# Kernel tuning notes

Hardware: AMD Instinct MI355X
Metric: run time of the kernel (lower is better)

## Reference

```python
import jax, jax.numpy as jnp
import numpy as np

LN_EPS = 1e-5  # torch nn.LayerNorm default eps


def _layernorm(x, g, b):
    m = jnp.mean(x, -1, keepdims=True)
    v = jnp.mean((x - m) ** 2, -1, keepdims=True)
    return (x - m) / jnp.sqrt(v + LN_EPS) * g + b


def _dw_causal_conv(x, w, bias=None):
    # x: (B, L, C); w: (C, K) depthwise kernels; causal via left-pad K-1
    C = x.shape[-1]
    K = w.shape[-1]
    xt = jnp.swapaxes(x, 1, 2)                       # (B, C, L)
    xp = jnp.pad(xt, ((0, 0), (0, 0), (K - 1, 0)))
    y = jax.lax.conv_general_dilated(
        xp, w[:, None, :], (1,), 'VALID',
        feature_group_count=C, dimension_numbers=('NCH', 'OIH', 'NCH'))
    if bias is not None:
        y = y + bias[None, :, None]
    return jnp.swapaxes(y, 1, 2)                     # (B, L, C)


def _s4d(x, Bp, Cp, log_dt, Dp):
    # Diagonal SSM: kernel K[l] = sum_n C[n]*dB[n]*dA[n]^l, shared across channels
    L, Dm = x.shape[1], x.shape[2]
    n = Bp.shape[0]
    A = -jnp.arange(1, n + 1, dtype=x.dtype)
    dt = jnp.clip(jnp.exp(log_dt), 1e-4, 1.0)
    dA = jnp.exp(jnp.clip(dt * A, -10.0, 10.0))                  # (n,)
    dB = (dA - 1.0) / jnp.minimum(A, -1e-4) * Bp                 # (n,)
    pows = dA[:, None] ** jnp.arange(L, dtype=x.dtype)[None, :]  # (n, L)
    Kk = jnp.nan_to_num((Cp * dB) @ pows, nan=0.0, posinf=0.0, neginf=0.0)  # (L,)
    y = _dw_causal_conv(x, jnp.broadcast_to(Kk[None, :], (Dm, L)))
    return y + Dp * x


def _mamba_block(x, g, b, W_in, cw, cb, sB, sC, ldt, sD, W_out, rs):
    res = x
    h = _layernorm(x, g, b)
    xz = h @ W_in.T                                  # (B, L, 2*d_inner)
    xp, z = jnp.split(xz, 2, axis=-1)
    xc = _dw_causal_conv(xp, cw, cb)                 # depthwise causal conv, k=4
    y = _s4d(xc, sB, sC, ldt, sD) * jax.nn.sigmoid(z)
    y = y @ W_out.T
    return res + jnp.clip(rs, 0.0, 1.5) * y          # dropout is identity in eval


def _forward(spatial_tokens_init, pos_embed, ln_g, ln_b, W_in, conv_w, conv_b,
             ssm_B, ssm_C, log_dt, ssm_D, W_out, res_scale, fin_g, fin_b,
             imp_W1, imp_b1, imp_W2, imp_b2, tex_W, tex_b, edge_W, edge_b,
             str_W, str_b):
    x = spatial_tokens_init + pos_embed
    for i in range(ln_g.shape[0]):  # fixed small layer count
        x = _mamba_block(x, ln_g[i], ln_b[i], W_in[i], conv_w[i], conv_b[i],
                         ssm_B[i], ssm_C[i], log_dt[i], ssm_D[i], W_out[i],
                         res_scale[i])
    tokens = _layernorm(x, fin_g, fin_b)
    # F.normalize(dim=-1, eps=1e-6)
    tn = tokens / jnp.maximum(jnp.sqrt(jnp.sum(tokens ** 2, -1, keepdims=True)), 1e-6)
    h = jax.nn.gelu(tn @ imp_W1.T + imp_b1, approximate=False)
    logits = (h @ imp_W2.T + imp_b2)[..., 0]
    w = jax.nn.softmax(logits, axis=-1)
    feats = jnp.sum(tokens * w[..., None], axis=1)
    return (feats,
            feats @ tex_W.T + tex_b,
            feats @ edge_W.T + edge_b,
            feats @ str_W.T + str_b,
            tokens, w)


B, N, D, DI, NL, NS, KC, DH = 512, 256, 128, 256, 4, 16, 4, 64
H = D // 2


def setup_inputs() -> dict:
    ks = jax.random.split(jax.random.key(0), 26)
    r = lambda k, sh, s=0.02: jax.random.normal(k, sh, dtype=jnp.float32) * s
    inp = {
        'spatial_tokens_init': jax.random.normal(ks[0], (B, N, D), dtype=jnp.float32),
        'pos_embed': r(ks[1], (1, N, D)),
        'ln_g': jnp.ones((NL, D), jnp.float32),
        'ln_b': jnp.zeros((NL, D), jnp.float32),
        'W_in': r(ks[2], (NL, 2 * DI, D)),
        'conv_w': r(ks[3], (NL, DI, KC), 0.2),
        'conv_b': r(ks[4], (NL, DI), 0.02),
        'ssm_B': r(ks[5], (NL, NS)),
        'ssm_C': r(ks[6], (NL, NS)),
        'log_dt': jax.random.uniform(ks[7], (NL,), jnp.float32,
                                     minval=float(np.log(1e-3)), maxval=float(np.log(0.1))),
        'ssm_D': jnp.zeros((NL,), jnp.float32),
        'W_out': r(ks[8], (NL, D, DI)),
        'res_scale': jnp.ones((NL,), jnp.float32),
        'fin_g': jnp.ones((D,), jnp.float32),
        'fin_b': jnp.zeros((D,), jnp.float32),
        'imp_W1': r(ks[9], (H, D)),
        'imp_b1': jnp.zeros((H,), jnp.float32),
        'imp_W2': r(ks[10], (1, H)),
        'imp_b2': jnp.zeros((1,), jnp.float32),
        'tex_W': r(ks[11], (DH, D)),
        'tex_b': jnp.zeros((DH,), jnp.float32),
        'edge_W': r(ks[12], (DH, D)),
        'edge_b': jnp.zeros((DH,), jnp.float32),
        'str_W': r(ks[13], (DH, D)),
        'str_b': jnp.zeros((DH,), jnp.float32),
    }
    return inp


def reference(spatial_tokens_init, pos_embed, ln_g, ln_b, W_in, conv_w, conv_b,
              ssm_B, ssm_C, log_dt, ssm_D, W_out, res_scale, fin_g, fin_b,
              imp_W1, imp_b1, imp_W2, imp_b2, tex_W, tex_b, edge_W, edge_b,
              str_W, str_b):
    return _forward(spatial_tokens_init, pos_embed, ln_g, ln_b, W_in, conv_w,
                    conv_b, ssm_B, ssm_C, log_dt, ssm_D, W_out, res_scale,
                    fin_g, fin_b, imp_W1, imp_b1, imp_W2, imp_b2, tex_W, tex_b,
                    edge_W, edge_b, str_W, str_b)
```

## Files before the change

kernel.cpp:

```cpp
#include <hip/hip_runtime.h>
#include <hip/hip_bf16.h>


typedef __bf16 bf16_8 __attribute__((ext_vector_type(8)));
typedef __bf16 bf16_4 __attribute__((ext_vector_type(4)));
typedef float  f32_4  __attribute__((ext_vector_type(4)));

#define LDKC 72

__global__ __launch_bounds__(256) void prep_kernel(const float* __restrict__ win,
                                                   const float* __restrict__ wout,
                                                   const float* __restrict__ w1,
                                                   __bf16* __restrict__ win16,
                                                   __bf16* __restrict__ wout16,
                                                   __bf16* __restrict__ w116) {
    int i = blockIdx.x * 256 + threadIdx.x;
    if (i < 4 * 512 * 128) win16[i] = (__bf16)win[i];
    if (i < 4 * 128 * 256) wout16[i] = (__bf16)wout[i];
    if (i < 64 * 128)      w116[i]  = (__bf16)w1[i];
}

__global__ __launch_bounds__(256) void build_T_kernel(const float* __restrict__ Bp,
                                                      const float* __restrict__ Cp,
                                                      const float* __restrict__ ldt,
                                                      const float* __restrict__ Dpv,
                                                      __bf16* __restrict__ Tg,
                                                      float* __restrict__ Rg) {
    __shared__ float rsum[4];
    int layer = blockIdx.y, l = blockIdx.x, j = threadIdx.x;
    int d = l - j;
    float val = 0.0f;
    if (d >= 0) {
        float dt = expf(ldt[layer]);
        dt = fminf(fmaxf(dt, 1e-4f), 1.0f);
        #pragma unroll
        for (int n = 0; n < 16; ++n) {
            float A = -(float)(n + 1);
            float e = fminf(fmaxf(dt * A, -10.0f), 10.0f);
            float dA = expf(e);
            float dB = (dA - 1.0f) / A * Bp[layer * 16 + n];
            val += Cp[layer * 16 + n] * dB * expf(e * (float)d);
        }
        if (d == 0) val += Dpv[layer];
    }
    __bf16 bv = (__bf16)val;
    Tg[layer * 65536 + l * 256 + j] = bv;
    float fv = (float)bv;
    #pragma unroll
    for (int o = 32; o; o >>= 1) fv += __shfl_xor(fv, o);
    int lane = j & 63, wave = j >> 6;
    if (lane == 0) rsum[wave] = fv;
    __syncthreads();
    if (j == 0) Rg[layer * 256 + l] = rsum[0] + rsum[1] + rsum[2] + rsum[3];
}

__global__ __launch_bounds__(256) void ln_first_kernel(const float* __restrict__ init,
                                                       const float* __restrict__ pos,
                                                       const float* __restrict__ g,
                                                       const float* __restrict__ bta,
                                                       float* __restrict__ x,
                                                       __bf16* __restrict__ h) {
    int wave = threadIdx.x >> 6, lane = threadIdx.x & 63;
    long tok = (long)blockIdx.x * 4 + wave;
    const float* xr = init + tok * 128;
    const float* pr = pos + (tok & 255) * 128;
    float v0 = xr[lane] + pr[lane];
    float v1 = xr[lane + 64] + pr[lane + 64];
    x[tok * 128 + lane]      = v0;
    x[tok * 128 + lane + 64] = v1;
    float s = v0 + v1, ss = v0 * v0 + v1 * v1;
    #pragma unroll
    for (int o = 32; o; o >>= 1) { s += __shfl_xor(s, o); ss += __shfl_xor(ss, o); }
    float m = s * (1.0f / 128.0f);
    float var = ss * (1.0f / 128.0f) - m * m;
    float r = rsqrtf(var + 1e-5f);
    __bf16* hr = h + tok * 128;
    hr[lane]      = (__bf16)((v0 - m) * r * g[lane]      + bta[lane]);
    hr[lane + 64] = (__bf16)((v1 - m) * r * g[lane + 64] + bta[lane + 64]);
}

__global__ __launch_bounds__(256) void gemm1_kernel(const __bf16* __restrict__ hmat,
                                                    const __bf16* __restrict__ win,
                                                    __bf16* __restrict__ xpt,
                                                    __bf16* __restrict__ z) {
    __shared__ __bf16 As[128 * LDKC];
    __shared__ __bf16 Bs[128 * LDKC];
    int tid = threadIdx.x;
    long m0 = (long)blockIdx.x * 128;
    int n0 = blockIdx.y * 128;
    int wave = tid >> 6, lane = tid & 63;
    int wm = wave >> 1, wn = wave & 1;
    int lrow = lane & 15, lk = (lane >> 4) * 8;
    f32_4 acc[4][4] = {};

    for (int kc = 0; kc < 2; ++kc) {
        const __bf16* asrc = hmat + m0 * 128 + kc * 64;
        const __bf16* bsrc = win + (long)n0 * 128 + kc * 64;
        #pragma unroll
        for (int i = 0; i < 4; ++i) {
            int idx = tid + i * 256;
            int row = idx >> 3, c4 = idx & 7;
            uint4 va = *(const uint4*)(asrc + row * 128 + c4 * 8);
            *(uint4*)(As + row * LDKC + c4 * 8) = va;
            uint4 vb = *(const uint4*)(bsrc + row * 128 + c4 * 8);
            *(uint4*)(Bs + row * LDKC + c4 * 8) = vb;
        }
        __syncthreads();
        #pragma unroll
        for (int kk = 0; kk < 64; kk += 32) {
            bf16_8 a[4], b[4];
            #pragma unroll
            for (int mt = 0; mt < 4; ++mt)
                a[mt] = *(const bf16_8*)(As + (wm * 64 + mt * 16 + lrow) * LDKC + kk + lk);
            #pragma unroll
            for (int nt = 0; nt < 4; ++nt)
                b[nt] = *(const bf16_8*)(Bs + (wn * 64 + nt * 16 + lrow) * LDKC + kk + lk);
            #pragma unroll
            for (int mt = 0; mt < 4; ++mt)
                #pragma unroll
                for (int nt = 0; nt < 4; ++nt)
                    acc[mt][nt] = __builtin_amdgcn_mfma_f32_16x16x32_bf16(
                        a[mt], b[nt], acc[mt][nt], 0, 0, 0);
        }
        __syncthreads();
    }

    int row_base = (lane >> 4) * 4;
    int col = lane & 15;
    if (n0 < 256) {
        #pragma unroll
        for (int mt = 0; mt < 4; ++mt) {
            long mg = m0 + wm * 64 + mt * 16 + row_base;
            int b = (int)(mg >> 8), l = (int)(mg & 255);
            #pragma unroll
            for (int nt = 0; nt < 4; ++nt) {
                int ng = n0 + wn * 64 + nt * 16 + col;
                bf16_4 o;
                #pragma unroll
                for (int r = 0; r < 4; ++r) o[r] = (__bf16)acc[mt][nt][r];
                *(bf16_4*)(xpt + (long)b * 65536 + (long)ng * 256 + l) = o;
            }
        }
    } else {
        int ncol0 = n0 - 256;
        #pragma unroll
        for (int mt = 0; mt < 4; ++mt) {
            long mg = m0 + wm * 64 + mt * 16 + row_base;
            #pragma unroll
            for (int nt = 0; nt < 4; ++nt) {
                int ng = ncol0 + wn * 64 + nt * 16 + col;
                #pragma unroll
                for (int r = 0; r < 4; ++r)
                    z[(mg + r) * 256 + ng] = (__bf16)acc[mt][nt][r];
            }
        }
    }
}

__global__ __launch_bounds__(512) void ssm_gemm_kernel(const __bf16* __restrict__ xct,
                                                       __bf16* __restrict__ zy,
                                                       const __bf16* __restrict__ Tg,
                                                       const float* __restrict__ Rg,
                                                       const float* __restrict__ cw,
                                                       const float* __restrict__ cb) {
    __shared__ __bf16 As[256 * LDKC];
    __shared__ __bf16 Bs[128 * LDKC];
    __shared__ float  bnd[3][128];
    __shared__ float  Rs[256];
    int tid = threadIdx.x;
    int batch = blockIdx.x >> 1;
    int ntile = blockIdx.x & 1;
    int c0 = ntile * 128;

    int wave = tid >> 6, lane = tid & 63;
    int wm = wave >> 2, wn = wave & 3;
    int lrow = lane & 15, lk = (lane >> 4) * 8;
    int quad = lane >> 4;
    f32_4 acc[8][2] = {};
    const __bf16* bsrc0 = xct + (long)batch * 65536 + (long)c0 * 256;

    if (tid < 256) Rs[tid] = Rg[tid];

    for (int kc = 0; kc < 4; ++kc) {
        int j0 = kc * 64;
        #pragma unroll
        for (int i = 0; i < 4; ++i) {
            int idx = tid + i * 512;
            int row = idx >> 3, c4 = idx & 7;
            uint4 va = *(const uint4*)(Tg + row * 256 + j0 + c4 * 8);
            *(uint4*)(As + row * LDKC + c4 * 8) = va;
        }
        #pragma unroll
        for (int i = 0; i < 2; ++i) {
            int idx = tid + i * 512;
            int row = idx >> 3, c4 = idx & 7;
            uint4 vb = *(const uint4*)(bsrc0 + (long)row * 256 + j0 + c4 * 8);
            *(uint4*)(Bs + row * LDKC + c4 * 8) = vb;
        }
        __syncthreads();
        #pragma unroll
        for (int kk = 0; kk < 64; kk += 32) {
            bf16_8 b0 = *(const bf16_8*)(Bs + (wn * 32 + lrow) * LDKC + kk + lk);
            bf16_8 b1 = *(const bf16_8*)(Bs + (wn * 32 + 16 + lrow) * LDKC + kk + lk);
            #pragma unroll
            for (int mt = 0; mt < 8; ++mt) {
                bf16_8 a = *(const bf16_8*)(As + (wm * 128 + mt * 16 + lrow) * LDKC + kk + lk);
                acc[mt][0] = __builtin_amdgcn_mfma_f32_16x16x32_bf16(a, b0, acc[mt][0], 0, 0, 0);
                acc[mt][1] = __builtin_amdgcn_mfma_f32_16x16x32_bf16(a, b1, acc[mt][1], 0, 0, 0);
            }
        }
        __syncthreads();
    }

    if (wm == 0 && quad == 3) {
        #pragma unroll
        for (int nt = 0; nt < 2; ++nt) {
            int colb = wn * 32 + nt * 16 + lrow;
            bnd[0][colb] = acc[7][nt][1];
            bnd[1][colb] = acc[7][nt][2];
            bnd[2][colb] = acc[7][nt][3];
        }
    }
    __syncthreads();

    float4 wv[2]; float cbv[2];
    #pragma unroll
    for (int nt = 0; nt < 2; ++nt) {
        int cg = c0 + wn * 32 + nt * 16 + lrow;
        wv[nt] = *(const float4*)(cw + cg * 4);
        cbv[nt] = cb[cg];
    }
    int src = (lane + 48) & 63;

    #pragma unroll
    for (int mt = 0; mt < 8; ++mt) {
        int lbase = wm * 128 + mt * 16 + quad * 4;
        int mp = mt > 0 ? mt - 1 : 0;
        float R0 = Rs[lbase], R1 = Rs[lbase + 1], R2 = Rs[lbase + 2], R3 = Rs[lbase + 3];
        #pragma unroll
        for (int nt = 0; nt < 2; ++nt) {
            int colb = wn * 32 + nt * 16 + lrow;
            int cg = c0 + colb;
            float s1 = __shfl(acc[mt][nt][3], src);
            float s2 = __shfl(acc[mt][nt][2], src);
            float s3 = __shfl(acc[mt][nt][1], src);
            float t1, t2, t3;
            if (mt == 0) {
                if (wm == 1) { t1 = bnd[2][colb]; t2 = bnd[1][colb]; t3 = bnd[0][colb]; }
                else         { t1 = 0.0f; t2 = 0.0f; t3 = 0.0f; }
            } else {
                t1 = __shfl(acc[mp][nt][3], src);
                t2 = __shfl(acc[mp][nt][2], src);
                t3 = __shfl(acc[mp][nt][1], src);
            }
            float pm1 = quad ? s1 : t1;
            float pm2 = quad ? s2 : t2;
            float pm3 = quad ? s3 : t3;
            float p0 = acc[mt][nt][0], p1 = acc[mt][nt][1];
            float p2 = acc[mt][nt][2], p3 = acc[mt][nt][3];
            float y0 = wv[nt].x * pm3 + wv[nt].y * pm2 + wv[nt].z * pm1 + wv[nt].w * p0 + cbv[nt] * R0;
            float y1 = wv[nt].x * pm2 + wv[nt].y * pm1 + wv[nt].z * p0  + wv[nt].w * p1 + cbv[nt] * R1;
            float y2 = wv[nt].x * pm1 + wv[nt].y * p0  + wv[nt].z * p1  + wv[nt].w * p2 + cbv[nt] * R2;
            float y3 = wv[nt].x * p0  + wv[nt].y * p1  + wv[nt].z * p2  + wv[nt].w * p3 + cbv[nt] * R3;
            long base = (long)batch * 65536 + (long)lbase * 256 + cg;
            float z0 = (float)zy[base];
            float z1 = (float)zy[base + 256];
            float z2 = (float)zy[base + 512];
            float z3 = (float)zy[base + 768];
            zy[base]       = (__bf16)(y0 / (1.0f + expf(-z0)));
            zy[base + 256] = (__bf16)(y1 / (1.0f + expf(-z1)));
            zy[base + 512] = (__bf16)(y2 / (1.0f + expf(-z2)));
            zy[base + 768] = (__bf16)(y3 / (1.0f + expf(-z3)));
        }
    }
}

__global__ __launch_bounds__(256) void gemm2_kernel(const __bf16* __restrict__ y,
                                                    const __bf16* __restrict__ wout,
                                                    float* __restrict__ x,
                                                    const float* __restrict__ rs_p,
                                                    const float* __restrict__ g,
                                                    const float* __restrict__ bta,
                                                    __bf16* __restrict__ hout,
                                                    float* __restrict__ tokens_out,
                                                    int final_mode) {
    __shared__ __bf16 As[128 * LDKC];
    __shared__ __bf16 Bs[128 * LDKC];
    __shared__ float s_sum[128][2];
    __shared__ float s_ssq[128][2];
    int tid = threadIdx.x;
    long m0 = (long)blockIdx.x * 128;
    int wave = tid >> 6, lane = tid & 63;
    int wm = wave >> 1, wn = wave & 1;
    int lrow = lane & 15, lk = (lane >> 4) * 8;
    f32_4 acc[4][4] = {};

    for (int kc = 0; kc < 4; ++kc) {
        const __bf16* asrc = y + m0 * 256 + kc * 64;
        const __bf16* bsrc = wout + kc * 64;
        #pragma unroll
        for (int i = 0; i < 4; ++i) {
            int idx = tid + i * 256;
            int row = idx >> 3, c4 = idx & 7;
            uint4 va = *(const uint4*)(asrc + row * 256 + c4 * 8);
            *(uint4*)(As + row * LDKC + c4 * 8) = va;
            uint4 vb = *(const uint4*)(bsrc + row * 256 + c4 * 8);
            *(uint4*)(Bs + row * LDKC + c4 * 8) = vb;
        }
        __syncthreads();
        #pragma unroll
        for (int kk = 0; kk < 64; kk += 32) {
            bf16_8 a[4], b[4];
            #pragma unroll
            for (int mt = 0; mt < 4; ++mt)
                a[mt] = *(const bf16_8*)(As + (wm * 64 + mt * 16 + lrow) * LDKC + kk + lk);
            #pragma unroll
            for (int nt = 0; nt < 4; ++nt)
                b[nt] = *(const bf16_8*)(Bs + (wn * 64 + nt * 16 + lrow) * LDKC + kk + lk);
            #pragma unroll
            for (int mt = 0; mt < 4; ++mt)
                #pragma unroll
                for (int nt = 0; nt < 4; ++nt)
                    acc[mt][nt] = __builtin_amdgcn_mfma_f32_16x16x32_bf16(
                        a[mt], b[nt], acc[mt][nt], 0, 0, 0);
        }
        __syncthreads();
    }

    float rs = rs_p[0];
    rs = fminf(fmaxf(rs, 0.0f), 1.5f);
    int quad = lane >> 4;
    int col = lane & 15;

    #pragma unroll
    for (int mt = 0; mt < 4; ++mt) {
        long mg = m0 + wm * 64 + mt * 16 + quad * 4;
        int tb = wm * 64 + mt * 16 + quad * 4;
        #pragma unroll
        for (int r = 0; r < 4; ++r) {
            float s = 0.0f, ss = 0.0f;
            #pragma unroll
            for (int nt = 0; nt < 4; ++nt) {
                int d = wn * 64 + nt * 16 + col;
                float xv = x[(mg + r) * 128 + d] + rs * acc[mt][nt][r];
                acc[mt][nt][r] = xv;
                s += xv; ss += xv * xv;
            }
            #pragma unroll
            for (int o = 8; o; o >>= 1) { s += __shfl_xor(s, o); ss += __shfl_xor(ss, o); }
            if (col == 0) {
                s_sum[tb + r][wn] = s;
                s_ssq[tb + r][wn] = ss;
            }
        }
    }
    __syncthreads();

    #pragma unroll
    for (int mt = 0; mt < 4; ++mt) {
        long mg = m0 + wm * 64 + mt * 16 + quad * 4;
        int tb = wm * 64 + mt * 16 + quad * 4;
        #pragma unroll
        for (int r = 0; r < 4; ++r) {
            float s  = s_sum[tb + r][0] + s_sum[tb + r][1];
            float ss = s_ssq[tb + r][0] + s_ssq[tb + r][1];
            float m = s * (1.0f / 128.0f);
            float var = ss * (1.0f / 128.0f) - m * m;
            float rstd = rsqrtf(var + 1e-5f);
            #pragma unroll
            for (int nt = 0; nt < 4; ++nt) {
                int d = wn * 64 + nt * 16 + col;
                float xv = acc[mt][nt][r];
                x[(mg + r) * 128 + d] = xv;
                float t = (xv - m) * rstd * g[d] + bta[d];
                if (!final_mode) {
                    hout[(mg + r) * 128 + d] = (__bf16)t;
                } else {
                    tokens_out[(mg + r) * 128 + d] = t;
                }
            }
        }
    }
}

__global__ __launch_bounds__(256) void l2n_kernel(const float* __restrict__ tokens,
                                                  __bf16* __restrict__ tn) {
    int wave = threadIdx.x >> 6, lane = threadIdx.x & 63;
    long tok = (long)blockIdx.x * 4 + wave;
    const float* tr = tokens + tok * 128;
    float t0 = tr[lane], t1 = tr[lane + 64];
    float q = t0 * t0 + t1 * t1;
    #pragma unroll
    for (int o = 32; o; o >>= 1) q += __shfl_xor(q, o);
    float inv = 1.0f / fmaxf(sqrtf(q), 1e-6f);
    tn[tok * 128 + lane]      = (__bf16)(t0 * inv);
    tn[tok * 128 + lane + 64] = (__bf16)(t1 * inv);
}

#define LDA 136
__global__ __launch_bounds__(256) void mlp_kernel(const __bf16* __restrict__ tn,
                                                  const __bf16* __restrict__ w1b,
                                                  const float* __restrict__ b1,
                                                  const float* __restrict__ W2,
                                                  const float* __restrict__ b2,
                                                  float* __restrict__ logits) {
    __shared__ __bf16 As[128 * LDA];
    __shared__ __bf16 Bs[64 * LDA];
    int tid = threadIdx.x;
    long m0 = (long)blockIdx.x * 128;
    const __bf16* asrc = tn + m0 * 128;
    #pragma unroll
    for (int i = 0; i < 8; ++i) {
        int idx = tid + i * 256;
        int row = idx >> 4, c = idx & 15;
        uint4 v = *(const uint4*)(asrc + row * 128 + c * 8);
        *(uint4*)(As + row * LDA + c * 8) = v;
    }
    #pragma unroll
    for (int i = 0; i < 4; ++i) {
        int idx = tid + i * 256;
        int row = idx >> 4, c = idx & 15;
        uint4 v = *(const uint4*)(w1b + row * 128 + c * 8);
        *(uint4*)(Bs + row * LDA + c * 8) = v;
    }
    __syncthreads();

    int wave = tid >> 6, lane = tid & 63;
    int lrow = lane & 15, lk = (lane >> 4) * 8;
    f32_4 acc[2][4] = {};
    #pragma unroll
    for (int kk = 0; kk < 128; kk += 32) {
        bf16_8 a[2], b[4];
        #pragma unroll
        for (int mt = 0; mt < 2; ++mt)
            a[mt] = *(const bf16_8*)(As + (wave * 32 + mt * 16 + lrow) * LDA + kk + lk);
        #pragma unroll
        for (int nt = 0; nt < 4; ++nt)
            b[nt] = *(const bf16_8*)(Bs + (nt * 16 + lrow) * LDA + kk + lk);
        #pragma unroll
        for (int mt = 0; mt < 2; ++mt)
            #pragma unroll
            for (int nt = 0; nt < 4; ++nt)
                acc[mt][nt] = __builtin_amdgcn_mfma_f32_16x16x32_bf16(
                    a[mt], b[nt], acc[mt][nt], 0, 0, 0);
    }

    int col = lane & 15, quad = lane >> 4;
    float b2v = b2[0];
    #pragma unroll
    for (int mt = 0; mt < 2; ++mt) {
        #pragma unroll
        for (int r = 0; r < 4; ++r) {
            float p = 0.0f;
            #pragma unroll
            for (int nt = 0; nt < 4; ++nt) {
                int jx = nt * 16 + col;
                float a = acc[mt][nt][r] + b1[jx];
                float gl = 0.5f * a * (1.0f + erff(a * 0.70710678118654752f));
                p += gl * W2[jx];
            }
            #pragma unroll
            for (int o = 8; o; o >>= 1) p += __shfl_xor(p, o);
            if (col == 0) {
                long tok = m0 + wave * 32 + mt * 16 + quad * 4 + r;
                logits[tok] = p + b2v;
            }
        }
    }
}

__global__ __launch_bounds__(256) void head_kernel(const float* __restrict__ tokens,
                                                   const float* __restrict__ logits,
                                                   const float* __restrict__ texW,
                                                   const float* __restrict__ texb,
                                                   const float* __restrict__ edgeW,
                                                   const float* __restrict__ edgeb,
                                                   const float* __restrict__ strW,
                                                   const float* __restrict__ strb,
                                                   float* __restrict__ feats_out,
                                                   float* __restrict__ tex_out,
                                                   float* __restrict__ edge_out,
                                                   float* __restrict__ str_out,
                                                   float* __restrict__ w_out) {
    __shared__ float wsm[256];
    __shared__ float red[8];
    __shared__ float feats_s[128];
    int b = blockIdx.x, tid = threadIdx.x;
    int lane = tid & 63, wave = tid >> 6;
    float lg = logits[(long)b * 256 + tid];
    float mx = lg;
    #pragma unroll
    for (int o = 32; o; o >>= 1) mx = fmaxf(mx, __shfl_xor(mx, o));
    if (lane == 0) red[wave] = mx;
    __syncthreads();
    float bm = fmaxf(fmaxf(red[0], red[1]), fmaxf(red[2], red[3]));
    float e = expf(lg - bm);
    float se = e;
    #pragma unroll
    for (int o = 32; o; o >>= 1) se += __shfl_xor(se, o);
    if (lane == 0) red[4 + wave] = se;
    __syncthreads();
    float tot = red[4] + red[5] + red[6] + red[7];
    float w = e / tot;
    wsm[tid] = w;
    w_out[(long)b * 256 + tid] = w;
    __syncthreads();
    if (tid < 128) {
        float acc = 0.0f;
        const float* tb = tokens + (long)b * 256 * 128 + tid;
        #pragma unroll 4
        for (int l = 0; l < 256; ++l) acc += tb[l * 128] * wsm[l];
        feats_s[tid] = acc;
        feats_out[(long)b * 128 + tid] = acc;
    }
    __syncthreads();
    if (tid < 192) {
        int head = tid >> 6, j = tid & 63;
        const float* W  = head == 0 ? texW : (head == 1 ? edgeW : strW);
        const float* bi = head == 0 ? texb : (head == 1 ? edgeb : strb);
        float* outp     = head == 0 ? tex_out : (head == 1 ? edge_out : str_out);
        const float* wr = W + j * 128;
        float acc = 0.0f;
        #pragma unroll 8
        for (int k = 0; k < 128; ++k) acc += feats_s[k] * wr[k];
        outp[(long)b * 64 + j] = acc + bi[j];
    }
}

extern "C" void kernel_launch(void* const* d_in, const int* in_sizes, int n_in,
                              void* d_out, int out_size, void* d_ws, size_t ws_size,
                              hipStream_t stream) {
    const float* init   = (const float*)d_in[0];
    const float* pos    = (const float*)d_in[1];
    const float* ln_g   = (const float*)d_in[2];
    const float* ln_b   = (const float*)d_in[3];
    const float* W_in   = (const float*)d_in[4];
    const float* conv_w = (const float*)d_in[5];
    const float* conv_b = (const float*)d_in[6];
    const float* ssm_B  = (const float*)d_in[7];
    const float* ssm_C  = (const float*)d_in[8];
    const float* log_dt = (const float*)d_in[9];
    const float* ssm_D  = (const float*)d_in[10];
    const float* W_out  = (const float*)d_in[11];
    const float* res_sc = (const float*)d_in[12];
    const float* fin_g  = (const float*)d_in[13];
    const float* fin_b  = (const float*)d_in[14];
    const float* imp_W1 = (const float*)d_in[15];
    const float* imp_b1 = (const float*)d_in[16];
    const float* imp_W2 = (const float*)d_in[17];
    const float* imp_b2 = (const float*)d_in[18];
    const float* tex_W  = (const float*)d_in[19];
    const float* tex_b  = (const float*)d_in[20];
    const float* edge_W = (const float*)d_in[21];
    const float* edge_b = (const float*)d_in[22];
    const float* str_W  = (const float*)d_in[23];
    const float* str_b  = (const float*)d_in[24];

    float* out = (float*)d_out;
    char* ws = (char*)d_ws;
    float*  x      = (float*)ws;
    __bf16* xpt    = (__bf16*)(ws + 67108864);
    __bf16* zb     = (__bf16*)(ws + 134217728);
    __bf16* hb     = (__bf16*)(ws + 201326592);
    __bf16* win16  = (__bf16*)(ws + 234881024);
    __bf16* wout16 = (__bf16*)(ws + 235405312);
    float*  logits = (float*)(ws + 235667456);
    __bf16* w1b    = (__bf16*)(ws + 236191744);
    __bf16* Tg     = (__bf16*)(ws + 236208128);
    float*  Rg     = (float*)(ws + 236732416);

    float* tokens = out + 163840;

    prep_kernel<<<1024, 256, 0, stream>>>(W_in, W_out, imp_W1, win16, wout16, w1b);
    build_T_kernel<<<dim3(256, 4), 256, 0, stream>>>(ssm_B, ssm_C, log_dt, ssm_D, Tg, Rg);
    ln_first_kernel<<<32768, 256, 0, stream>>>(init, pos, ln_g, ln_b, x, hb);
    for (int l = 0; l < 4; ++l) {
        gemm1_kernel<<<dim3(1024, 4), 256, 0, stream>>>(hb, win16 + l * 65536, xpt, zb);
        ssm_gemm_kernel<<<1024, 512, 0, stream>>>(xpt, zb, Tg + l * 65536, Rg + l * 256,
                                                  conv_w + l * 1024, conv_b + l * 256);
        int fin = (l == 3);
        const float* gn = fin ? fin_g : ln_g + (l + 1) * 128;
        const float* bn = fin ? fin_b : ln_b + (l + 1) * 128;
        gemm2_kernel<<<1024, 256, 0, stream>>>(zb, wout16 + l * 32768, x, res_sc + l,
                                               gn, bn, hb, fin ? tokens : nullptr, fin);
    }
    __bf16* tn = hb;
    l2n_kernel<<<32768, 256, 0, stream>>>(tokens, tn);
    mlp_kernel<<<1024, 256, 0, stream>>>(tn, w1b, imp_b1, imp_W2, imp_b2, logits);
    head_kernel<<<512, 256, 0, stream>>>(tokens, logits, tex_W, tex_b, edge_W, edge_b,
                                         str_W, str_b, out, out + 65536, out + 98304,
                                         out + 131072, out + 16941056);
}
```

Baseline: 857.5 us.

## Use direct global-to-LDS loads with XOR swizzle and vectorize LN kernels

Replaces the register-staged global-to-shared tile copies in the three GEMM kernels with global_load_lds 16-byte direct loads into an unpadded, XOR-swizzled LDS layout, and adjusts the MFMA fragment reads to match the swizzle. The aim is to cut VGPR traffic and the extra LDS writes, and to avoid bank conflicts without padding. The first-layer LayerNorm and L2-normalize kernels are also vectorized to float4 with two tokens per wave, which halves the grid size. The risk is that the swizzle mapping or the per-lane LDS placement of global_load_lds is wrong, and the loads are still synchronous with no overlap.

```diff
diff --git a/kernel.cpp b/kernel.cpp
--- a/kernel.cpp
+++ b/kernel.cpp
@@ -6,7 +6,9 @@
 typedef __bf16 bf16_4 __attribute__((ext_vector_type(4)));
 typedef float  f32_4  __attribute__((ext_vector_type(4)));
 
-#define LDKC 72
+#define GLOAD16(src, dst) __builtin_amdgcn_global_load_lds( \
+    (const __attribute__((address_space(1))) void*)(src),   \
+    (__attribute__((address_space(3))) void*)(dst), 16, 0, 0)
 
 __global__ __launch_bounds__(256) void prep_kernel(const float* __restrict__ win,
                                                    const float* __restrict__ wout,
@@ -54,67 +56,73 @@
     if (j == 0) Rg[layer * 256 + l] = rsum[0] + rsum[1] + rsum[2] + rsum[3];
 }
 
-__global__ __launch_bounds__(256) void ln_first_kernel(const float* __restrict__ init,
-                                                       const float* __restrict__ pos,
+__global__ __launch_bounds__(256) void ln_first_kernel(const float4* __restrict__ init4,
+                                                       const float4* __restrict__ pos4,
                                                        const float* __restrict__ g,
                                                        const float* __restrict__ bta,
-                                                       float* __restrict__ x,
+                                                       float4* __restrict__ x4,
                                                        __bf16* __restrict__ h) {
-    int wave = threadIdx.x >> 6, lane = threadIdx.x & 63;
-    long tok = (long)blockIdx.x * 4 + wave;
-    const float* xr = init + tok * 128;
-    const float* pr = pos + (tok & 255) * 128;
-    float v0 = xr[lane] + pr[lane];
-    float v1 = xr[lane + 64] + pr[lane + 64];
-    x[tok * 128 + lane]      = v0;
-    x[tok * 128 + lane + 64] = v1;
-    float s = v0 + v1, ss = v0 * v0 + v1 * v1;
-    #pragma unroll
-    for (int o = 32; o; o >>= 1) { s += __shfl_xor(s, o); ss += __shfl_xor(ss, o); }
+    int tid = threadIdx.x;
+    int wave = tid >> 6, lane = tid & 63;
+    int half = lane >> 5, l32 = lane & 31;
+    long tok = (long)blockIdx.x * 8 + wave * 2 + half;
+    float4 v = init4[tok * 32 + l32];
+    float4 p = pos4[(tok & 255) * 32 + l32];
+    v.x += p.x; v.y += p.y; v.z += p.z; v.w += p.w;
+    x4[tok * 32 + l32] = v;
+    float s = v.x + v.y + v.z + v.w;
+    float ss = v.x * v.x + v.y * v.y + v.z * v.z + v.w * v.w;
+    #pragma unroll
+    for (int o = 16; o; o >>= 1) { s += __shfl_xor(s, o); ss += __shfl_xor(ss, o); }
     float m = s * (1.0f / 128.0f);
     float var = ss * (1.0f / 128.0f) - m * m;
     float r = rsqrtf(var + 1e-5f);
-    __bf16* hr = h + tok * 128;
-    hr[lane]      = (__bf16)((v0 - m) * r * g[lane]      + bta[lane]);
-    hr[lane + 64] = (__bf16)((v1 - m) * r * g[lane + 64] + bta[lane + 64]);
+    bf16_4 hv;
+    int d0 = l32 * 4;
+    hv[0] = (__bf16)((v.x - m) * r * g[d0]     + bta[d0]);
+    hv[1] = (__bf16)((v.y - m) * r * g[d0 + 1] + bta[d0 + 1]);
+    hv[2] = (__bf16)((v.z - m) * r * g[d0 + 2] + bta[d0 + 2]);
+    hv[3] = (__bf16)((v.w - m) * r * g[d0 + 3] + bta[d0 + 3]);
+    *(bf16_4*)(h + tok * 128 + d0) = hv;
 }
 
 __global__ __launch_bounds__(256) void gemm1_kernel(const __bf16* __restrict__ hmat,
                                                     const __bf16* __restrict__ win,
                                                     __bf16* __restrict__ xpt,
                                                     __bf16* __restrict__ z) {
-    __shared__ __bf16 As[128 * LDKC];
-    __shared__ __bf16 Bs[128 * LDKC];
+    __shared__ __align__(16) __bf16 As[128 * 64];
+    __shared__ __align__(16) __bf16 Bs[128 * 64];
     int tid = threadIdx.x;
     long m0 = (long)blockIdx.x * 128;
     int n0 = blockIdx.y * 128;
     int wave = tid >> 6, lane = tid & 63;
     int wm = wave >> 1, wn = wave & 1;
     int lrow = lane & 15, lk = (lane >> 4) * 8;
+    int r7 = lrow & 7;
+    int rl = lane >> 3, sl = lane & 7;
+    int scol = ((sl ^ rl) << 3);
     f32_4 acc[4][4] = {};
 
     for (int kc = 0; kc < 2; ++kc) {
         const __bf16* asrc = hmat + m0 * 128 + kc * 64;
         const __bf16* bsrc = win + (long)n0 * 128 + kc * 64;
         #pragma unroll
-        for (int i = 0; i < 4; ++i) {
-            int idx = tid + i * 256;
-            int row = idx >> 3, c4 = idx & 7;
-            uint4 va = *(const uint4*)(asrc + row * 128 + c4 * 8);
-            *(uint4*)(As + row * LDKC + c4 * 8) = va;
-            uint4 vb = *(const uint4*)(bsrc + row * 128 + c4 * 8);
-            *(uint4*)(Bs + row * LDKC + c4 * 8) = vb;
+        for (int j = 0; j < 4; ++j) {
+            int chunk = wave * 4 + j;
+            GLOAD16(asrc + (long)(chunk * 8 + rl) * 128 + scol, As + chunk * 512);
+            GLOAD16(bsrc + (long)(chunk * 8 + rl) * 128 + scol, Bs + chunk * 512);
         }
         __syncthreads();
         #pragma unroll
         for (int kk = 0; kk < 64; kk += 32) {
+            int sw = ((((kk + lk) >> 3) ^ r7) << 3);
             bf16_8 a[4], b[4];
             #pragma unroll
             for (int mt = 0; mt < 4; ++mt)
-                a[mt] = *(const bf16_8*)(As + (wm * 64 + mt * 16 + lrow) * LDKC + kk + lk);
+                a[mt] = *(const bf16_8*)(As + (wm * 64 + mt * 16 + lrow) * 64 + sw);
             #pragma unroll
             for (int nt = 0; nt < 4; ++nt)
-                b[nt] = *(const bf16_8*)(Bs + (wn * 64 + nt * 16 + lrow) * LDKC + kk + lk);
+                b[nt] = *(const bf16_8*)(Bs + (wn * 64 + nt * 16 + lrow) * 64 + sw);
             #pragma unroll
             for (int mt = 0; mt < 4; ++mt)
                 #pragma unroll
@@ -163,8 +171,8 @@
                                                        const float* __restrict__ Rg,
                                                        const float* __restrict__ cw,
                                                        const float* __restrict__ cb) {
-    __shared__ __bf16 As[256 * LDKC];
-    __shared__ __bf16 Bs[128 * LDKC];
+    __shared__ __align__(16) __bf16 As[256 * 64];
+    __shared__ __align__(16) __bf16 Bs[128 * 64];
     __shared__ float  bnd[3][128];
     __shared__ float  Rs[256];
     int tid = threadIdx.x;
@@ -175,7 +183,10 @@
     int wave = tid >> 6, lane = tid & 63;
     int wm = wave >> 2, wn = wave & 3;
     int lrow = lane & 15, lk = (lane >> 4) * 8;
+    int r7 = lrow & 7;
     int quad = lane >> 4;
+    int rl = lane >> 3, sl = lane & 7;
+    int scol = ((sl ^ rl) << 3);
     f32_4 acc[8][2] = {};
     const __bf16* bsrc0 = xct + (long)batch * 65536 + (long)c0 * 256;
 
@@ -183,28 +194,27 @@
 
     for (int kc = 0; kc < 4; ++kc) {
         int j0 = kc * 64;
-        #pragma unroll
-        for (int i = 0; i < 4; ++i) {
-            int idx = tid + i * 512;
-            int row = idx >> 3, c4 = idx & 7;
-            uint4 va = *(const uint4*)(Tg + row * 256 + j0 + c4 * 8);
-            *(uint4*)(As + row * LDKC + c4 * 8) = va;
-        }
-        #pragma unroll
-        for (int i = 0; i < 2; ++i) {
-            int idx = tid + i * 512;
-            int row = idx >> 3, c4 = idx & 7;
-            uint4 vb = *(const uint4*)(bsrc0 + (long)row * 256 + j0 + c4 * 8);
-            *(uint4*)(Bs + row * LDKC + c4 * 8) = vb;
+        const __bf16* asrc = Tg + j0;
+        const __bf16* bsrc = bsrc0 + j0;
+        #pragma unroll
+        for (int j = 0; j < 4; ++j) {
+            int chunk = wave * 4 + j;
+            GLOAD16(asrc + (long)(chunk * 8 + rl) * 256 + scol, As + chunk * 512);
+        }
+        #pragma unroll
+        for (int j = 0; j < 2; ++j) {
+            int chunk = wave * 2 + j;
+            GLOAD16(bsrc + (long)(chunk * 8 + rl) * 256 + scol, Bs + chunk * 512);
         }
         __syncthreads();
         #pragma unroll
         for (int kk = 0; kk < 64; kk += 32) {
-            bf16_8 b0 = *(const bf16_8*)(Bs + (wn * 32 + lrow) * LDKC + kk + lk);
-            bf16_8 b1 = *(const bf16_8*)(Bs + (wn * 32 + 16 + lrow) * LDKC + kk + lk);
+            int sw = ((((kk + lk) >> 3) ^ r7) << 3);
+            bf16_8 b0 = *(const bf16_8*)(Bs + (wn * 32 + lrow) * 64 + sw);
+            bf16_8 b1 = *(const bf16_8*)(Bs + (wn * 32 + 16 + lrow) * 64 + sw);
             #pragma unroll
             for (int mt = 0; mt < 8; ++mt) {
-                bf16_8 a = *(const bf16_8*)(As + (wm * 128 + mt * 16 + lrow) * LDKC + kk + lk);
+                bf16_8 a = *(const bf16_8*)(As + (wm * 128 + mt * 16 + lrow) * 64 + sw);
                 acc[mt][0] = __builtin_amdgcn_mfma_f32_16x16x32_bf16(a, b0, acc[mt][0], 0, 0, 0);
                 acc[mt][1] = __builtin_amdgcn_mfma_f32_16x16x32_bf16(a, b1, acc[mt][1], 0, 0, 0);
             }
@@ -284,8 +294,8 @@
                                                     __bf16* __restrict__ hout,
                                                     float* __restrict__ tokens_out,
                                                     int final_mode) {
-    __shared__ __bf16 As[128 * LDKC];
-    __shared__ __bf16 Bs[128 * LDKC];
+    __shared__ __align__(16) __bf16 As[128 * 64];
+    __shared__ __align__(16) __bf16 Bs[128 * 64];
     __shared__ float s_sum[128][2];
     __shared__ float s_ssq[128][2];
     int tid = threadIdx.x;
@@ -293,30 +303,31 @@
     int wave = tid >> 6, lane = tid & 63;
     int wm = wave >> 1, wn = wave & 1;
     int lrow = lane & 15, lk = (lane >> 4) * 8;
+    int r7 = lrow & 7;
+    int rl = lane >> 3, sl = lane & 7;
+    int scol = ((sl ^ rl) << 3);
     f32_4 acc[4][4] = {};
 
     for (int kc = 0; kc < 4; ++kc) {
         const __bf16* asrc = y + m0 * 256 + kc * 64;
         const __bf16* bsrc = wout + kc * 64;
         #pragma unroll
-        for (int i = 0; i < 4; ++i) {
-            int idx = tid + i * 256;
-            int row = idx >> 3, c4 = idx & 7;
-            uint4 va = *(const uint4*)(asrc + row * 256 + c4 * 8);
-            *(uint4*)(As + row * LDKC + c4 * 8) = va;
-            uint4 vb = *(const uint4*)(bsrc + row * 256 + c4 * 8);
-            *(uint4*)(Bs + row * LDKC + c4 * 8) = vb;
+        for (int j = 0; j < 4; ++j) {
+            int chunk = wave * 4 + j;
+            GLOAD16(asrc + (long)(chunk * 8 + rl) * 256 + scol, As + chunk * 512);
+            GLOAD16(bsrc + (long)(chunk * 8 + rl) * 256 + scol, Bs + chunk * 512);
         }
         __syncthreads();
         #pragma unroll
         for (int kk = 0; kk < 64; kk += 32) {
+            int sw = ((((kk + lk) >> 3) ^ r7) << 3);
             bf16_8 a[4], b[4];
             #pragma unroll
             for (int mt = 0; mt < 4; ++mt)
-                a[mt] = *(const bf16_8*)(As + (wm * 64 + mt * 16 + lrow) * LDKC + kk + lk);
+                a[mt] = *(const bf16_8*)(As + (wm * 64 + mt * 16 + lrow) * 64 + sw);
             #pragma unroll
             for (int nt = 0; nt < 4; ++nt)
-                b[nt] = *(const bf16_8*)(Bs + (wn * 64 + nt * 16 + lrow) * LDKC + kk + lk);
+                b[nt] = *(const bf16_8*)(Bs + (wn * 64 + nt * 16 + lrow) * 64 + sw);
             #pragma unroll
             for (int mt = 0; mt < 4; ++mt)
                 #pragma unroll
@@ -383,18 +394,21 @@
     }
 }
 
-__global__ __launch_bounds__(256) void l2n_kernel(const float* __restrict__ tokens,
+__global__ __launch_bounds__(256) void l2n_kernel(const float4* __restrict__ tokens4,
                                                   __bf16* __restrict__ tn) {
-    int wave = threadIdx.x >> 6, lane = threadIdx.x & 63;
-    long tok = (long)blockIdx.x * 4 + wave;
-    const float* tr = tokens + tok * 128;
-    float t0 = tr[lane], t1 = tr[lane + 64];
-    float q = t0 * t0 + t1 * t1;
-    #pragma unroll
-    for (int o = 32; o; o >>= 1) q += __shfl_xor(q, o);
+    int tid = threadIdx.x;
+    int wave = tid >> 6, lane = tid & 63;
+    int half = lane >> 5, l32 = lane & 31;
+    long tok = (long)blockIdx.x * 8 + wave * 2 + half;
+    float4 t = tokens4[tok * 32 + l32];
+    float q = t.x * t.x + t.y * t.y + t.z * t.z + t.w * t.w;
+    #pragma unroll
+    for (int o = 16; o; o >>= 1) q += __shfl_xor(q, o);
     float inv = 1.0f / fmaxf(sqrtf(q), 1e-6f);
-    tn[tok * 128 + lane]      = (__bf16)(t0 * inv);
-    tn[tok * 128 + lane + 64] = (__bf16)(t1 * inv);
+    bf16_4 o4;
+    o4[0] = (__bf16)(t.x * inv); o4[1] = (__bf16)(t.y * inv);
+    o4[2] = (__bf16)(t.z * inv); o4[3] = (__bf16)(t.w * inv);
+    *(bf16_4*)(tn + tok * 128 + l32 * 4) = o4;
 }
 
 #define LDA 136
@@ -573,7 +587,8 @@
 
     prep_kernel<<<1024, 256, 0, stream>>>(W_in, W_out, imp_W1, win16, wout16, w1b);
     build_T_kernel<<<dim3(256, 4), 256, 0, stream>>>(ssm_B, ssm_C, log_dt, ssm_D, Tg, Rg);
-    ln_first_kernel<<<32768, 256, 0, stream>>>(init, pos, ln_g, ln_b, x, hb);
+    ln_first_kernel<<<16384, 256, 0, stream>>>((const float4*)init, (const float4*)pos,
+                                               ln_g, ln_b, (float4*)x, hb);
     for (int l = 0; l < 4; ++l) {
         gemm1_kernel<<<dim3(1024, 4), 256, 0, stream>>>(hb, win16 + l * 65536, xpt, zb);
         ssm_gemm_kernel<<<1024, 512, 0, stream>>>(xpt, zb, Tg + l * 65536, Rg + l * 256,
@@ -585,7 +600,7 @@
                                                gn, bn, hb, fin ? tokens : nullptr, fin);
     }
     __bf16* tn = hb;
-    l2n_kernel<<<32768, 256, 0, stream>>>(tokens, tn);
+    l2n_kernel<<<16384, 256, 0, stream>>>((const float4*)tokens, tn);
     mlp_kernel<<<1024, 256, 0, stream>>>(tn, w1b, imp_b1, imp_W2, imp_b2, logits);
     head_kernel<<<512, 256, 0, stream>>>(tokens, logits, tex_W, tex_b, edge_W, edge_b,
                                          str_W, str_b, out, out + 65536, out + 98304,
```

Result: faster. 827.2 us (-3.5%).
